# Kernel optimization log

Measured on AMD Instinct MI355X. Metric: run time of the kernel, lower is better.

## Reference

```python
import jax, jax.numpy as jnp
import numpy as np

BATCH = 8192
NUM_FEATURES = 2048
NUM_CLASSES = 10
NUM_LAYERS = 2
LOGIT_SCALE = 5.0
INV_SQRT2 = 1.0 / np.sqrt(2.0)


def setup_inputs() -> dict:
    key = jax.random.key(0)
    k1, k2 = jax.random.split(key)
    # input feature phases in [-pi, pi), one oscillator thread per feature
    x = jax.random.uniform(k1, (BATCH, NUM_FEATURES), jnp.float32, -np.pi, np.pi)
    # trainable phase shifts: (num_stacks * num_layers * num_features,) ~ U(-pi, pi)
    weights = jax.random.uniform(k2, (NUM_LAYERS * NUM_FEATURES,), jnp.float32, -np.pi, np.pi)
    return {"x": x, "weights": weights}


def _vpc_forward(x, weights):
    # x: (B, N) phases; state z_i = e^{i x_i} with unit amplitude
    B, N = x.shape
    w = weights.reshape(NUM_LAYERS, N)  # per-layer shift parameters
    z = jnp.exp(1j * x)  # complex64 state vector, shape (B, N)
    for layer in range(NUM_LAYERS):
        # shift: rotate every thread phase by its trainable weight
        z = z * jnp.exp(1j * w[layer])  # broadcast (N,) over batch
        # mix: Hadamard-like 2x2 unitary on adjacent pairs (0,1),(2,3),...
        a = z[:, 0::2]
        b = z[:, 1::2]
        z = jnp.stack(((a + b) * INV_SQRT2, (a - b) * INV_SQRT2), axis=-1).reshape(B, N)
        # dft: global unitary DFT across the N threads
        z = jnp.fft.fft(z, norm="ortho")
    phases = jnp.arctan2(jnp.imag(z), jnp.real(z))  # (B, N)
    # multi-class readout: sin-smoothed phases of first K threads -> softmax
    logits = jnp.sin(phases[:, :NUM_CLASSES]) * LOGIT_SCALE
    return jax.nn.softmax(logits, axis=-1)  # (B, K)


def reference(x, weights):
    return _vpc_forward(x, weights)
```

## Files before the change

### kernel.cpp

```cpp
#include <hip/hip_runtime.h>
#include <math.h>

#define NF       2048
#define NC       10
#define THREADS  256

__device__ __forceinline__ int swz(int i) { return i ^ (((i >> 4) & 7) << 1); }

__device__ __forceinline__ float2 cadd(float2 a, float2 b){ return make_float2(a.x+b.x, a.y+b.y); }
__device__ __forceinline__ float2 csub(float2 a, float2 b){ return make_float2(a.x-b.x, a.y-b.y); }
__device__ __forceinline__ float2 cmul(float2 a, float2 b){
    return make_float2(a.x*b.x - a.y*b.y, a.x*b.y + a.y*b.x);
}
__device__ __forceinline__ float2 mul_mi(float2 d){ return make_float2(d.y, -d.x); }
__device__ __forceinline__ float2 mul_w1(float2 d){
    const float C = 0.70710678118654752f;
    return make_float2(C*(d.x + d.y), C*(d.y - d.x));
}
__device__ __forceinline__ float2 mul_w3(float2 d){
    const float C = 0.70710678118654752f;
    return make_float2(C*(d.y - d.x), -C*(d.x + d.y));
}

template<int S>
__device__ __forceinline__ void stage8_ip(float2* __restrict__ buf,
                                          const float2* __restrict__ twl,
                                          int tid, int rbase)
{
    __syncthreads();
    float2 a0 = buf[rbase       ];
    float2 a1 = buf[rbase +  256];
    float2 a2 = buf[rbase +  512];
    float2 a3 = buf[rbase +  768];
    float2 a4 = buf[rbase + 1024];
    float2 a5 = buf[rbase + 1280];
    float2 a6 = buf[rbase + 1536];
    float2 a7 = buf[rbase + 1792];
    const int q  = tid & (S - 1);
    const int pb = tid ^ q;
    float2 w1 = twl[pb];
    __syncthreads();
    float2 u0 = cadd(a0,a4), u1 = csub(a0,a4);
    float2 u2 = cadd(a1,a5), u3 = mul_w1(csub(a1,a5));
    float2 u4 = cadd(a2,a6), u5 = mul_mi(csub(a2,a6));
    float2 u6 = cadd(a3,a7), u7 = mul_w3(csub(a3,a7));
    float2 v0 = cadd(u0,u4), v2 = csub(u0,u4);
    float2 v1 = cadd(u1,u5), v3 = csub(u1,u5);
    float2 v4 = cadd(u2,u6), v6 = mul_mi(csub(u2,u6));
    float2 v5 = cadd(u3,u7), v7 = mul_mi(csub(u3,u7));
    const int base = q + 8 * pb;
    {
        float2 y0 = cadd(cadd(u0,u4), cadd(u2,u6));
        buf[swz(base)] = y0;
    }
    float2 v4b = cadd(u2,u6);
    float2 y4 = csub(v0,v4b);
    float2 w2 = cmul(w1,w1);
    float2 w4 = cmul(w2,w2);
    buf[swz(base + 4*S)] = cmul(y4,w4);
    float2 y1 = cadd(v1,v5), y5 = csub(v1,v5);
    buf[swz(base +   S)] = cmul(y1,w1);
    float2 w5 = cmul(w4,w1);
    buf[swz(base + 5*S)] = cmul(y5,w5);
    float2 y2 = cadd(v2,v6), y6 = csub(v2,v6);
    buf[swz(base + 2*S)] = cmul(y2,w2);
    float2 w6 = cmul(w4,w2);
    buf[swz(base + 6*S)] = cmul(y6,w6);
    float2 y3 = cadd(v3,v7), y7 = csub(v3,v7);
    float2 w3 = cmul(w2,w1);
    buf[swz(base + 3*S)] = cmul(y3,w3);
    float2 w7 = cmul(w4,w3);
    buf[swz(base + 7*S)] = cmul(y7,w7);
}

__device__ __forceinline__ void stage4_rot_ip(float2* __restrict__ buf,
                                              const float2* __restrict__ w1r,
                                              int tid, int r2base)
{
    __syncthreads();
    float4 R0 = *(const float4*)&buf[r2base       ];
    float4 R1 = *(const float4*)&buf[r2base +  512];
    float4 R2 = *(const float4*)&buf[r2base + 1024];
    float4 R3 = *(const float4*)&buf[r2base + 1536];
    float2 u0 = make_float2(R0.x,R0.y), v0 = make_float2(R0.z,R0.w);
    float2 u1 = make_float2(R1.x,R1.y), v1 = make_float2(R1.z,R1.w);
    float2 u2 = make_float2(R2.x,R2.y), v2 = make_float2(R2.z,R2.w);
    float2 u3 = make_float2(R3.x,R3.y), v3 = make_float2(R3.z,R3.w);
    float2 us0 = cadd(u0,u2), us1 = cadd(u1,u3);
    float2 ud0 = csub(u0,u2), ud1 = mul_mi(csub(u1,u3));
    float2 vs0 = cadd(v0,v2), vs1 = cadd(v1,v3);
    float2 vd0 = csub(v0,v2), vd1 = mul_mi(csub(v1,v3));
    float2 uy[4] = { cadd(us0,us1), cadd(ud0,ud1), csub(us0,us1), csub(ud0,ud1) };
    float2 vy[4] = { cadd(vs0,vs1), cadd(vd0,vd1), csub(vs0,vs1), csub(vd0,vd1) };
    #pragma unroll
    for (int k = 0; k < 4; ++k) {
        float2 wv = w1r[tid + 256*k];
        float s0, c0, s1, c1;
        __sincosf(wv.x, &s0, &c0);
        __sincosf(wv.y, &s1, &c1);
        float2 z0 = cmul(uy[k], make_float2(c0,s0));
        float2 z1 = cmul(vy[k], make_float2(c1,s1));
        *(float4*)&buf[r2base + 512*k] =
            make_float4(z0.x+z1.x, z0.y+z1.y, z0.x-z1.x, z0.y-z1.y);
    }
}

__global__ __launch_bounds__(THREADS, 6) void vpc_kernel(
        const float* __restrict__ x, const float* __restrict__ w,
        float* __restrict__ out) {
    __shared__ __align__(16) float2 A[NF];
    __shared__ __align__(16) float2 twl[256];
    __shared__ float  smax[NC];
    const int tid   = threadIdx.x;
    const int row   = blockIdx.x;
    const int rbase  = swz(tid);
    const int r2base = swz(2*tid);

    {
        float a = -(float)tid * (float)(M_PI / 1024.0);
        float s, c;
        __sincosf(a, &s, &c);
        twl[tid] = make_float2(c, s);
    }

    const float4* xr4 = (const float4*)(x + (size_t)row * NF);
    const float4* wr4 = (const float4*)w;
    #pragma unroll
    for (int i = 0; i < 2; ++i) {
        const int g = tid + 256*i;
        float4 xv = xr4[g];
        float4 wv = wr4[g];
        float s0,c0,s1,c1,s2,c2,s3,c3;
        __sincosf(xv.x + wv.x, &s0, &c0);
        __sincosf(xv.y + wv.y, &s1, &c1);
        __sincosf(xv.z + wv.z, &s2, &c2);
        __sincosf(xv.w + wv.w, &s3, &c3);
        *(float4*)&A[swz(4*g)]     = make_float4(c0+c1, s0+s1, c0-c1, s0-s1);
        *(float4*)&A[swz(4*g + 2)] = make_float4(c2+c3, s2+s3, c2-c3, s2-s3);
    }

    stage8_ip<1> (A, twl, tid, rbase);
    stage8_ip<8> (A, twl, tid, rbase);
    stage8_ip<64>(A, twl, tid, rbase);
    stage4_rot_ip(A, (const float2*)(w + NF), tid, r2base);

    stage8_ip<1> (A, twl, tid, rbase);
    stage8_ip<8> (A, twl, tid, rbase);
    stage8_ip<64>(A, twl, tid, rbase);

    __syncthreads();
    if (tid < NC) {
        float2 a0 = A[tid];
        float2 a1 = A[tid + 512];
        float2 a2 = A[tid + 1024];
        float2 a3 = A[tid + 1536];
        float2 y = cadd(cadd(a0,a2), cadd(a1,a3));
        float mag = sqrtf(y.x*y.x + y.y*y.y);
        smax[tid] = 5.0f * y.y / fmaxf(mag, 1e-30f);
    }
    __syncthreads();
    if (tid < NC) {
        float l = smax[tid];
        float mx = smax[0];
        #pragma unroll
        for (int j = 1; j < NC; ++j) mx = fmaxf(mx, smax[j]);
        float s = 0.f;
        #pragma unroll
        for (int j = 0; j < NC; ++j) s += __expf(smax[j] - mx);
        out[(size_t)row * NC + tid] = __expf(l - mx) / s;
    }
}

extern "C" void kernel_launch(void* const* d_in, const int* in_sizes, int n_in,
                              void* d_out, int out_size, void* d_ws, size_t ws_size,
                              hipStream_t stream) {
    const float* x = (const float*)d_in[0];
    const float* w = (const float*)d_in[1];
    float* out = (float*)d_out;
    (void)d_ws; (void)ws_size;

    vpc_kernel<<<8192, THREADS, 0, stream>>>(x, w, out);
}
```

Baseline: 126.7 us.

## Prune final FFT to the ten output bins and raise occupancy bound

Since only the first ten FFT outputs are needed, the second FFT now runs one full radix-8 stage, then a truncated stage computing only the outputs feeding bins 0-15. The last stage is replaced by a 32-term serial sum over shared memory in the ten readout threads. The stage8 butterfly also reuses already-computed partial sums, and the launch-bounds occupancy hint rises from 6 to 8 blocks. The serial 32-element reduction on ten threads adds latency at the tail and may leave lanes idle.

```diff
diff --git a/kernel.cpp b/kernel.cpp
--- a/kernel.cpp
+++ b/kernel.cpp
@@ -49,12 +49,8 @@
     float2 v4 = cadd(u2,u6), v6 = mul_mi(csub(u2,u6));
     float2 v5 = cadd(u3,u7), v7 = mul_mi(csub(u3,u7));
     const int base = q + 8 * pb;
-    {
-        float2 y0 = cadd(cadd(u0,u4), cadd(u2,u6));
-        buf[swz(base)] = y0;
-    }
-    float2 v4b = cadd(u2,u6);
-    float2 y4 = csub(v0,v4b);
+    buf[swz(base)] = cadd(v0,v4);
+    float2 y4 = csub(v0,v4);
     float2 w2 = cmul(w1,w1);
     float2 w4 = cmul(w2,w2);
     buf[swz(base + 4*S)] = cmul(y4,w4);
@@ -71,6 +67,37 @@
     buf[swz(base + 3*S)] = cmul(y3,w3);
     float2 w7 = cmul(w4,w3);
     buf[swz(base + 7*S)] = cmul(y7,w7);
+}
+
+__device__ __forceinline__ void stage8_trunc(float2* __restrict__ buf,
+                                             const float2* __restrict__ twl,
+                                             int tid, int rbase)
+{
+    __syncthreads();
+    float2 a0 = buf[rbase       ];
+    float2 a1 = buf[rbase +  256];
+    float2 a2 = buf[rbase +  512];
+    float2 a3 = buf[rbase +  768];
+    float2 a4 = buf[rbase + 1024];
+    float2 a5 = buf[rbase + 1280];
+    float2 a6 = buf[rbase + 1536];
+    float2 a7 = buf[rbase + 1792];
+    const int q  = tid & 7;
+    const int pb = tid ^ q;
+    float2 w1 = twl[pb];
+    __syncthreads();
+    const int base = q + 8 * pb;
+    float2 y0 = cadd(cadd(cadd(a0,a4), cadd(a2,a6)),
+                     cadd(cadd(a1,a5), cadd(a3,a7)));
+    buf[swz(base)] = y0;
+    if (q < 2) {
+        float2 u1 = csub(a0,a4);
+        float2 u3 = mul_w1(csub(a1,a5));
+        float2 u5 = mul_mi(csub(a2,a6));
+        float2 u7 = mul_w3(csub(a3,a7));
+        float2 y1 = cadd(cadd(u1,u5), cadd(u3,u7));
+        buf[swz(base + 8)] = cmul(y1, w1);
+    }
 }
 
 __device__ __forceinline__ void stage4_rot_ip(float2* __restrict__ buf,
@@ -105,7 +132,7 @@
     }
 }
 
-__global__ __launch_bounds__(THREADS, 6) void vpc_kernel(
+__global__ __launch_bounds__(THREADS, 8) void vpc_kernel(
         const float* __restrict__ x, const float* __restrict__ w,
         float* __restrict__ out) {
     __shared__ __align__(16) float2 A[NF];
@@ -144,19 +171,19 @@
     stage8_ip<64>(A, twl, tid, rbase);
     stage4_rot_ip(A, (const float2*)(w + NF), tid, r2base);
 
-    stage8_ip<1> (A, twl, tid, rbase);
-    stage8_ip<8> (A, twl, tid, rbase);
-    stage8_ip<64>(A, twl, tid, rbase);
+    stage8_ip<1>(A, twl, tid, rbase);
+    stage8_trunc(A, twl, tid, rbase);
 
     __syncthreads();
     if (tid < NC) {
-        float2 a0 = A[tid];
-        float2 a1 = A[tid + 512];
-        float2 a2 = A[tid + 1024];
-        float2 a3 = A[tid + 1536];
-        float2 y = cadd(cadd(a0,a2), cadd(a1,a3));
-        float mag = sqrtf(y.x*y.x + y.y*y.y);
-        smax[tid] = 5.0f * y.y / fmaxf(mag, 1e-30f);
+        float2 acc = make_float2(0.f, 0.f);
+        #pragma unroll 8
+        for (int r = 0; r < 32; ++r) {
+            int addr = (tid + 64*r) ^ ((r & 1) << 3);
+            acc = cadd(acc, A[addr]);
+        }
+        float mag = sqrtf(acc.x*acc.x + acc.y*acc.y);
+        smax[tid] = 5.0f * acc.y / fmaxf(mag, 1e-30f);
     }
     __syncthreads();
     if (tid < NC) {
```

Result: no change. 125.2 us (-1.2%).
